# Kernel tuning notes

Hardware: AMD Instinct MI355X
Metric: run time of the kernel (lower is better)

Reference implementation:

```python
import jax, jax.numpy as jnp
import numpy as np

N_NODES = 50000
N_EDGES = 1600000
N_GRAPHS = 512
IN_SIZE = 44
HIDDEN = 256
CONV_NUMS = 3


def setup_inputs() -> dict:
    key = jax.random.key(0)
    ks = jax.random.split(key, 10)
    h = jax.random.normal(ks[0], (N_NODES, IN_SIZE), dtype=jnp.float32)
    src = jax.random.randint(ks[1], (N_EDGES,), 0, N_NODES)
    dst = jax.random.randint(ks[2], (N_EDGES,), 0, N_NODES)
    graph_ids = jnp.sort(jax.random.randint(ks[3], (N_NODES,), 0, N_GRAPHS))
    # learned params (kaiming-ish scale)
    W_proj = jax.random.normal(ks[4], (IN_SIZE, HIDDEN), dtype=jnp.float32) * (2.0 / IN_SIZE) ** 0.5
    b_proj = jnp.zeros((HIDDEN,), dtype=jnp.float32)
    W_lin = jax.random.normal(ks[5], (HIDDEN, HIDDEN), dtype=jnp.float32) * (2.0 / HIDDEN) ** 0.5
    b_lin = jnp.zeros((HIDDEN,), dtype=jnp.float32)
    W_out = jax.random.normal(ks[6], (HIDDEN * CONV_NUMS, HIDDEN), dtype=jnp.float32) * (2.0 / (HIDDEN * CONV_NUMS)) ** 0.5
    b_out = jnp.zeros((HIDDEN,), dtype=jnp.float32)
    return {"h": h, "src": src, "dst": dst, "graph_ids": graph_ids,
            "W_proj": W_proj, "b_proj": b_proj, "W_lin": W_lin, "b_lin": b_lin,
            "W_out": W_out, "b_out": b_out}


def reference(h, src, dst, graph_ids, W_proj, b_proj, W_lin, b_lin, W_out, b_out):
    # initial projection
    h = h @ W_proj + b_proj  # [N, HIDDEN]
    # in-degree for mean aggregation (nodes with 0 in-edges get 0 aggregate)
    ones_e = jnp.ones((src.shape[0],), dtype=h.dtype)
    deg = jax.ops.segment_sum(ones_e, dst, num_segments=N_NODES)  # [N]
    inv_deg = jnp.where(deg > 0, 1.0 / jnp.maximum(deg, 1.0), 0.0)[:, None]
    outs = []
    for _ in range(CONV_NUMS):
        # DGL GINConv(mean, eps=0): h' = linear(h + mean_{u in N(v)} h_u)
        agg = jax.ops.segment_sum(h[src], dst, num_segments=N_NODES) * inv_deg
        h = (h + agg) @ W_lin + b_lin  # shared linear across layers
        outs.append(h)
    res = jnp.concatenate(outs, axis=1) @ W_out + b_out  # [N, HIDDEN]
    # dgl.mean_nodes: per-graph mean readout
    cnt = jax.ops.segment_sum(jnp.ones((N_NODES,), dtype=res.dtype), graph_ids, num_segments=N_GRAPHS)
    g_sum = jax.ops.segment_sum(res, graph_ids, num_segments=N_GRAPHS)
    return g_sum / jnp.maximum(cnt, 1.0)[:, None]
```

## Files before the change

### kernel.cpp

```cpp
#include <hip/hip_runtime.h>
#include <hip/hip_fp8.h>

#define N_NODES   50000
#define N_EDGES   1600000
#define N_GRAPHS  512
#define IN_SIZE   44
#define HIDDEN    256
#define CONV_NUMS 3
#define NBK       ((N_NODES + 255) / 256)
#define XK        48

typedef __attribute__((ext_vector_type(8))) short short8v;
typedef __attribute__((ext_vector_type(4))) float f32x4;

__device__ __forceinline__ float bf2f(unsigned short u) {
    return __uint_as_float(((unsigned int)u) << 16);
}
__device__ __forceinline__ unsigned short f2bf(float f) {
    unsigned int u = __float_as_uint(f);
    unsigned int r = (u + 0x7fffu + ((u >> 16) & 1u)) >> 16;
    return (unsigned short)r;
}

#if __has_builtin(__builtin_amdgcn_cvt_f32_fp8)
template <int SEL>
__device__ __forceinline__ float fp8tof(unsigned int w) {
    return __builtin_amdgcn_cvt_f32_fp8((int)w, SEL);
}
#else
template <int SEL>
__device__ __forceinline__ float fp8tof(unsigned int w) {
    __hip_fp8_e4m3 q;
    q.__x = (__hip_fp8_storage_t)((w >> (SEL * 8)) & 0xff);
    return (float)q;
}
#endif

#if __has_builtin(__builtin_amdgcn_cvt_pk_fp8_f32)
__device__ __forceinline__ unsigned int pk4fp8(float f0, float f1, float f2, float f3) {
    int lo = __builtin_amdgcn_cvt_pk_fp8_f32(f0, f1, 0, false);
    return (unsigned int)__builtin_amdgcn_cvt_pk_fp8_f32(f2, f3, lo, true);
}
#else
__device__ __forceinline__ unsigned int pk4fp8(float f0, float f1, float f2, float f3) {
    __hip_fp8_e4m3 a(f0), b(f1), c(f2), d(f3);
    return (unsigned int)a.__x | ((unsigned int)b.__x << 8) |
           ((unsigned int)c.__x << 16) | ((unsigned int)d.__x << 24);
}
#endif

__device__ __forceinline__ unsigned char f2fp8(float f) {
    return (unsigned char)(pk4fp8(f, 0.f, 0.f, 0.f) & 0xff);
}

__global__ __launch_bounds__(256) void k_passA(const int* __restrict__ dst,
                                               const int* __restrict__ gid,
                                               int* __restrict__ bucket_cnt,
                                               int* __restrict__ gcnt) {
    __shared__ int hb[NBK];
    __shared__ int hg[N_GRAPHS];
    int tid = threadIdx.x;
    for (int i = tid; i < NBK; i += 256) hb[i] = 0;
    for (int i = tid; i < N_GRAPHS; i += 256) hg[i] = 0;
    __syncthreads();
    int t = blockIdx.x * 256 + tid;
    int stride = gridDim.x * 256;
    for (int e = t; e < N_EDGES; e += stride) atomicAdd(&hb[dst[e] >> 8], 1);
    for (int v = t; v < N_NODES; v += stride) atomicAdd(&hg[gid[v]], 1);
    __syncthreads();
    for (int i = tid; i < NBK; i += 256) if (hb[i]) atomicAdd(&bucket_cnt[i], hb[i]);
    for (int i = tid; i < N_GRAPHS; i += 256) if (hg[i]) atomicAdd(&gcnt[i], hg[i]);
}

__global__ void k_bscan(const int* __restrict__ bucket_cnt, int* __restrict__ bucket_base,
                        int* __restrict__ bucket_cursor, int* __restrict__ row_ptr) {
    __shared__ int s[256];
    int t = threadIdx.x;
    int v = (t < NBK) ? bucket_cnt[t] : 0;
    s[t] = v;
    __syncthreads();
    for (int off = 1; off < 256; off <<= 1) {
        int a = (t >= off) ? s[t - off] : 0;
        __syncthreads();
        s[t] += a;
        __syncthreads();
    }
    if (t < NBK) {
        int base = s[t] - v;
        bucket_base[t] = base;
        bucket_cursor[t] = base;
    }
    if (t == 0) {
        bucket_base[NBK] = N_EDGES;
        row_ptr[N_NODES] = N_EDGES;
    }
}

#define BCH 8192
__global__ __launch_bounds__(256) void k_passB(const int* __restrict__ src,
                                               const int* __restrict__ dst,
                                               int* __restrict__ bucket_cursor,
                                               int* __restrict__ pairs) {
    __shared__ int hist[NBK];
    __shared__ int excl[NBK];
    __shared__ int cur[NBK];
    __shared__ int gbase[NBK];
    __shared__ int lp[BCH];
    __shared__ int sc[256];
    int tid = threadIdx.x;
    int e0 = blockIdx.x * BCH;
    int cnt = min(BCH, N_EDGES - e0);
    for (int i = tid; i < NBK; i += 256) hist[i] = 0;
    __syncthreads();
    for (int i = tid; i < cnt; i += 256) atomicAdd(&hist[dst[e0 + i] >> 8], 1);
    __syncthreads();
    int hv = (tid < NBK) ? hist[tid] : 0;
    sc[tid] = hv;
    __syncthreads();
    for (int off = 1; off < 256; off <<= 1) {
        int a = (tid >= off) ? sc[tid - off] : 0;
        __syncthreads();
        sc[tid] += a;
        __syncthreads();
    }
    if (tid < NBK) {
        excl[tid] = sc[tid] - hv;
        cur[tid]  = sc[tid] - hv;
    }
    __syncthreads();
    for (int i = tid; i < cnt; i += 256) {
        int d = dst[e0 + i];
        int b = d >> 8;
        int pos = atomicAdd(&cur[b], 1);
        lp[pos] = (b << 24) | ((d & 255) << 16) | src[e0 + i];
    }
    __syncthreads();
    if (tid < NBK && hist[tid] > 0)
        gbase[tid] = atomicAdd(&bucket_cursor[tid], hist[tid]);
    __syncthreads();
    for (int i = tid; i < cnt; i += 256) {
        int p = lp[i];
        int b = (p >> 24) & 0xff;
        pairs[gbase[b] + (i - excl[b])] = p;
    }
}

__global__ __launch_bounds__(256) void k_passC(const int* __restrict__ pairs,
                                               const int* __restrict__ bucket_base,
                                               int* __restrict__ row_ptr,
                                               unsigned short* __restrict__ colu) {
    __shared__ int hist[256];
    __shared__ int cur[256];
    __shared__ int sc[256];
    int b = blockIdx.x;
    int tid = threadIdx.x;
    int v0 = b << 8;
    int e0 = bucket_base[b], e1 = bucket_base[b + 1];
    hist[tid] = 0;
    __syncthreads();
    for (int i = e0 + tid; i < e1; i += 256) atomicAdd(&hist[(pairs[i] >> 16) & 0xff], 1);
    __syncthreads();
    int hv = hist[tid];
    sc[tid] = hv;
    __syncthreads();
    for (int off = 1; off < 256; off <<= 1) {
        int a = (tid >= off) ? sc[tid - off] : 0;
        __syncthreads();
        sc[tid] += a;
        __syncthreads();
    }
    int base = e0 + sc[tid] - hv;
    int v = v0 + tid;
    if (v < N_NODES) row_ptr[v] = base;
    cur[tid] = base;
    __syncthreads();
    for (int i = e0 + tid; i < e1; i += 256) {
        int p = pairs[i];
        int pos = atomicAdd(&cur[(p >> 16) & 0xff], 1);
        colu[pos] = (unsigned short)(p & 0xffff);
    }
}

__global__ __launch_bounds__(256) void k_prep(const float* __restrict__ Wl,
                                              const float* __restrict__ Wproj,
                                              const float* __restrict__ X,
                                              unsigned short* __restrict__ WlPack,
                                              unsigned short* __restrict__ WprojPack,
                                              unsigned short* __restrict__ Xb,
                                              unsigned char* __restrict__ Xb8) {
    int b = blockIdx.x;
    int tid = threadIdx.x;
    if (b < 32) {
        int i = b * 256 + tid;
        int kg = i >> 8, n = i & 255;
        short8v v;
#pragma unroll
        for (int j = 0; j < 8; j++) v[j] = (short)f2bf(Wl[(kg * 8 + j) * HIDDEN + n]);
        *(short8v*)(WlPack + (size_t)(kg * 256 + n) * 8) = v;
    } else if (b < 40) {
        int i = (b - 32) * 256 + tid;
        int kg = i >> 8, n = i & 255;
        short8v v;
#pragma unroll
        for (int j = 0; j < 8; j++) {
            int k = kg * 8 + j;
            v[j] = (k < IN_SIZE) ? (short)f2bf(Wproj[k * HIDDEN + n]) : (short)0;
        }
        *(short8v*)(WprojPack + (size_t)(kg * 256 + n) * 8) = v;
    } else {
        const int TOT = N_NODES * XK;
        int id0 = (b - 40) * 2048 + tid;
#pragma unroll
        for (int j = 0; j < 8; j++) {
            int id = id0 + j * 256;
            if (id < TOT) {
                int row = id / XK, c = id % XK;
                float val = (c < IN_SIZE) ? X[row * IN_SIZE + c] : 0.f;
                Xb[id]  = f2bf(val);
                Xb8[id] = f2fp8(val);
            }
        }
    }
}

__device__ __forceinline__ int rsplit(const int* rp, int s0, int len, int k) {
    if (k >= 8) return 64;
    int t = s0 + (int)(((long long)len * k) >> 3);
    int lo = 0, hi = 64;
    while (lo < hi) {
        int mid = (lo + hi) >> 1;
        if (rp[mid] < t) lo = mid + 1; else hi = mid;
    }
    return lo;
}

#define TLS 264
#define K1S 72
__global__ __launch_bounds__(512, 8) void k_layer1(const unsigned short* __restrict__ Xb,
                                                   const unsigned char* __restrict__ Xb8,
                                                   const int* __restrict__ row_ptr,
                                                   const unsigned short* __restrict__ colu,
                                                   const unsigned short* __restrict__ WprojPack,
                                                   const float* __restrict__ bp,
                                                   const unsigned short* __restrict__ WlPack,
                                                   const float* __restrict__ bl,
                                                   const int* __restrict__ gid,
                                                   unsigned short* __restrict__ hout,
                                                   unsigned char* __restrict__ hout8,
                                                   float* __restrict__ GsumL) {
    __shared__ unsigned short tl[64 * TLS];
    unsigned short* tl1 = tl;
    __shared__ float bpm[64];
    __shared__ int gl[64];
    __shared__ int rp[65];
    int tid = threadIdx.x;
    int w = tid >> 6, lane = tid & 63, quad = lane >> 4, l16 = lane & 15;
    int m0 = blockIdx.x * 64;

    if (tid < 65) rp[tid] = row_ptr[min(m0 + tid, N_NODES)];
    if (tid < 64) gl[tid] = (m0 + tid < N_NODES) ? gid[m0 + tid] : -1;
    __syncthreads();
    int s0 = rp[0], len = rp[64] - s0;
    int rlo = rsplit(rp, s0, len, w), rhi = rsplit(rp, s0, len, w + 1);

    for (int r = rlo; r < rhi; r++) {
        int v = m0 + r;
        float a0 = 0.f, a1 = 0.f;
        float val = 0.f;
        float mul = 1.f;
        if (v < N_NODES) {
            int s = rp[r], e = rp[r + 1];
            if (lane < XK) {
                int i = s;
                for (; i + 8 <= e; i += 8) {
                    int u0 = colu[i],     u1 = colu[i + 1];
                    int u2 = colu[i + 2], u3 = colu[i + 3];
                    int u4 = colu[i + 4], u5 = colu[i + 5];
                    int u6 = colu[i + 6], u7 = colu[i + 7];
                    unsigned int t0 = Xb8[u0 * XK + lane];
                    unsigned int t1 = Xb8[u1 * XK + lane];
                    unsigned int t2 = Xb8[u2 * XK + lane];
                    unsigned int t3 = Xb8[u3 * XK + lane];
                    unsigned int t4 = Xb8[u4 * XK + lane];
                    unsigned int t5 = Xb8[u5 * XK + lane];
                    unsigned int t6 = Xb8[u6 * XK + lane];
                    unsigned int t7 = Xb8[u7 * XK + lane];
                    a0 += (fp8tof<0>(t0) + fp8tof<0>(t1)) + (fp8tof<0>(t2) + fp8tof<0>(t3));
                    a1 += (fp8tof<0>(t4) + fp8tof<0>(t5)) + (fp8tof<0>(t6) + fp8tof<0>(t7));
                }
                for (; i + 2 <= e; i += 2) {
                    a0 += fp8tof<0>((unsigned int)Xb8[colu[i] * XK + lane]);
                    a1 += fp8tof<0>((unsigned int)Xb8[colu[i + 1] * XK + lane]);
                }
                if (i < e) a0 += fp8tof<0>((unsigned int)Xb8[colu[i] * XK + lane]);
            }
            float inv = 0.f;
            if (e > s) { inv = 1.0f / (float)(e - s); mul = 2.f; }
            float self = (lane < XK) ? bf2f(Xb[(size_t)v * XK + lane]) : 0.f;
            val = self + inv * (a0 + a1);
        }
        tl1[r * K1S + lane] = (lane < XK) ? f2bf(val) : (unsigned short)0;
        if (lane == 0) bpm[r] = mul;
    }
    __syncthreads();

    int n0 = w * 32;
    f32x4 acc[4][2];
#pragma unroll
    for (int mt = 0; mt < 4; mt++) {
        acc[mt][0] = (f32x4){0.f, 0.f, 0.f, 0.f};
        acc[mt][1] = (f32x4){0.f, 0.f, 0.f, 0.f};
    }
#pragma unroll
    for (int ks = 0; ks < 2; ks++) {
        int kg = ks * 4 + quad;
        short8v bfr0 = *(const short8v*)(WprojPack + (size_t)(kg * 256 + n0 + l16) * 8);
        short8v bfr1 = *(const short8v*)(WprojPack + (size_t)(kg * 256 + n0 + 16 + l16) * 8);
#pragma unroll
        for (int mt = 0; mt < 4; mt++) {
            short8v afr = *(const short8v*)(tl1 + (mt * 16 + l16) * K1S + ks * 32 + quad * 8);
            acc[mt][0] = __builtin_amdgcn_mfma_f32_16x16x32_bf16(afr, bfr0, acc[mt][0], 0, 0, 0);
            acc[mt][1] = __builtin_amdgcn_mfma_f32_16x16x32_bf16(afr, bfr1, acc[mt][1], 0, 0, 0);
        }
    }
    __syncthreads();
#pragma unroll
    for (int nt = 0; nt < 2; nt++) {
        int colg = n0 + nt * 16 + l16;
        float bb = bp[colg];
#pragma unroll
        for (int mt = 0; mt < 4; mt++)
#pragma unroll
            for (int r = 0; r < 4; r++) {
                int row = mt * 16 + quad * 4 + r;
                tl[row * TLS + colg] = f2bf(acc[mt][nt][r] + bb * bpm[row]);
            }
    }
    __syncthreads();

#pragma unroll
    for (int mt = 0; mt < 4; mt++) {
        acc[mt][0] = (f32x4){0.f, 0.f, 0.f, 0.f};
        acc[mt][1] = (f32x4){0.f, 0.f, 0.f, 0.f};
    }
#pragma unroll
    for (int ks = 0; ks < 8; ks++) {
        int kg = ks * 4 + quad;
        short8v bfr0 = *(const short8v*)(WlPack + (size_t)(kg * 256 + n0 + l16) * 8);
        short8v bfr1 = *(const short8v*)(WlPack + (size_t)(kg * 256 + n0 + 16 + l16) * 8);
#pragma unroll
        for (int mt = 0; mt < 4; mt++) {
            short8v afr = *(const short8v*)(tl + (mt * 16 + l16) * TLS + ks * 32 + quad * 8);
            acc[mt][0] = __builtin_amdgcn_mfma_f32_16x16x32_bf16(afr, bfr0, acc[mt][0], 0, 0, 0);
            acc[mt][1] = __builtin_amdgcn_mfma_f32_16x16x32_bf16(afr, bfr1, acc[mt][1], 0, 0, 0);
        }
    }
    __syncthreads();

#pragma unroll
    for (int nt = 0; nt < 2; nt++) {
        int colg = n0 + nt * 16 + l16;
        float bb = bl[colg];
#pragma unroll
        for (int mt = 0; mt < 4; mt++)
#pragma unroll
            for (int r = 0; r < 4; r++)
                tl[(mt * 16 + quad * 4 + r) * TLS + colg] = f2bf(acc[mt][nt][r] + bb);
    }
    __syncthreads();

    for (int i = tid; i < 64 * 64; i += 512) {
        int r = i >> 6, c4 = i & 63;
        int v = m0 + r;
        if (v < N_NODES) {
            ushort4 q = *(ushort4*)(tl + r * TLS + c4 * 4);
            ((ushort4*)hout)[(size_t)v * 64 + c4] = q;
            ((unsigned int*)hout8)[(size_t)v * 64 + c4] =
                pk4fp8(bf2f(q.x), bf2f(q.y), bf2f(q.z), bf2f(q.w));
        }
    }
    {
        int c = tid & 255;
        int r0 = (tid >> 8) * 32;
        float a2 = 0.f;
        int curg = gl[r0];
        for (int r = r0; r < r0 + 32; r++) {
            int g = gl[r];
            if (g < 0) break;
            if (g != curg) {
                atomicAdd(&GsumL[curg * HIDDEN + c], a2);
                a2 = 0.f;
                curg = g;
            }
            a2 += bf2f(tl[r * TLS + c]);
        }
        if (curg >= 0) atomicAdd(&GsumL[curg * HIDDEN + c], a2);
    }
}

__global__ __launch_bounds__(512, 8) void k_layer(const unsigned short* __restrict__ h,
                                                  const unsigned char* __restrict__ h8,
                                                  const int* __restrict__ row_ptr,
                                                  const unsigned short* __restrict__ colu,
                                                  const unsigned short* __restrict__ Wpack,
                                                  const float* __restrict__ bias,
                                                  const int* __restrict__ gid,
                                                  unsigned short* __restrict__ hout,
                                                  unsigned char* __restrict__ hout8,
                                                  int write8,
                                                  float* __restrict__ GsumL) {
    __shared__ unsigned short tl[64 * TLS];
    __shared__ int gl[64];
    __shared__ int rp[65];
    int tid = threadIdx.x;
    int w = tid >> 6, lane = tid & 63, quad = lane >> 4, l16 = lane & 15;
    int m0 = blockIdx.x * 64;

    if (tid < 65) rp[tid] = row_ptr[min(m0 + tid, N_NODES)];
    if (tid < 64) gl[tid] = (m0 + tid < N_NODES) ? gid[m0 + tid] : -1;
    __syncthreads();
    int s0 = rp[0], len = rp[64] - s0;
    int rlo = rsplit(rp, s0, len, w), rhi = rsplit(rp, s0, len, w + 1);

    const unsigned int* h8v = (const unsigned int*)h8;
    const ushort4* hv = (const ushort4*)h;
    for (int r = rlo; r < rhi; r++) {
        int v = m0 + r;
        float a0 = 0.f, a1 = 0.f, a2 = 0.f, a3 = 0.f;
        if (v < N_NODES) {
            int s = rp[r], e = rp[r + 1];
            int i = s;
            for (; i + 8 <= e; i += 8) {
                int u0 = colu[i],     u1 = colu[i + 1];
                int u2 = colu[i + 2], u3 = colu[i + 3];
                int u4 = colu[i + 4], u5 = colu[i + 5];
                int u6 = colu[i + 6], u7 = colu[i + 7];
                unsigned int p0 = h8v[(size_t)u0 * 64 + lane];
                unsigned int p1 = h8v[(size_t)u1 * 64 + lane];
                unsigned int p2 = h8v[(size_t)u2 * 64 + lane];
                unsigned int p3 = h8v[(size_t)u3 * 64 + lane];
                unsigned int p4 = h8v[(size_t)u4 * 64 + lane];
                unsigned int p5 = h8v[(size_t)u5 * 64 + lane];
                unsigned int p6 = h8v[(size_t)u6 * 64 + lane];
                unsigned int p7 = h8v[(size_t)u7 * 64 + lane];
                a0 += (fp8tof<0>(p0) + fp8tof<0>(p1)) + (fp8tof<0>(p2) + fp8tof<0>(p3))
                    + (fp8tof<0>(p4) + fp8tof<0>(p5)) + (fp8tof<0>(p6) + fp8tof<0>(p7));
                a1 += (fp8tof<1>(p0) + fp8tof<1>(p1)) + (fp8tof<1>(p2) + fp8tof<1>(p3))
                    + (fp8tof<1>(p4) + fp8tof<1>(p5)) + (fp8tof<1>(p6) + fp8tof<1>(p7));
                a2 += (fp8tof<2>(p0) + fp8tof<2>(p1)) + (fp8tof<2>(p2) + fp8tof<2>(p3))
                    + (fp8tof<2>(p4) + fp8tof<2>(p5)) + (fp8tof<2>(p6) + fp8tof<2>(p7));
                a3 += (fp8tof<3>(p0) + fp8tof<3>(p1)) + (fp8tof<3>(p2) + fp8tof<3>(p3))
                    + (fp8tof<3>(p4) + fp8tof<3>(p5)) + (fp8tof<3>(p6) + fp8tof<3>(p7));
            }
            for (; i + 4 <= e; i += 4) {
                int u0 = colu[i], u1 = colu[i + 1], u2 = colu[i + 2], u3 = colu[i + 3];
                unsigned int p0 = h8v[(size_t)u0 * 64 + lane];
                unsigned int p1 = h8v[(size_t)u1 * 64 + lane];
                unsigned int p2 = h8v[(size_t)u2 * 64 + lane];
                unsigned int p3 = h8v[(size_t)u3 * 64 + lane];
                a0 += (fp8tof<0>(p0) + fp8tof<0>(p1)) + (fp8tof<0>(p2) + fp8tof<0>(p3));
                a1 += (fp8tof<1>(p0) + fp8tof<1>(p1)) + (fp8tof<1>(p2) + fp8tof<1>(p3));
                a2 += (fp8tof<2>(p0) + fp8tof<2>(p1)) + (fp8tof<2>(p2) + fp8tof<2>(p3));
                a3 += (fp8tof<3>(p0) + fp8tof<3>(p1)) + (fp8tof<3>(p2) + fp8tof<3>(p3));
            }
            for (; i < e; i++) {
                unsigned int p = h8v[(size_t)colu[i] * 64 + lane];
                a0 += fp8tof<0>(p); a1 += fp8tof<1>(p);
                a2 += fp8tof<2>(p); a3 += fp8tof<3>(p);
            }
            float inv = (e > s) ? 1.0f / (float)(e - s) : 0.0f;
            ushort4 hs = hv[(size_t)v * 64 + lane];
            a0 = bf2f(hs.x) + inv * a0;
            a1 = bf2f(hs.y) + inv * a1;
            a2 = bf2f(hs.z) + inv * a2;
            a3 = bf2f(hs.w) + inv * a3;
        }
        ushort4 o;
        o.x = f2bf(a0); o.y = f2bf(a1); o.z = f2bf(a2); o.w = f2bf(a3);
        *(ushort4*)(tl + r * TLS + lane * 4) = o;
    }
    __syncthreads();

    int n0 = w * 32;
    f32x4 acc[4][2];
#pragma unroll
    for (int mt = 0; mt < 4; mt++) {
        acc[mt][0] = (f32x4){0.f, 0.f, 0.f, 0.f};
        acc[mt][1] = (f32x4){0.f, 0.f, 0.f, 0.f};
    }
#pragma unroll
    for (int ks = 0; ks < 8; ks++) {
        int kg = ks * 4 + quad;
        short8v bfr0 = *(const short8v*)(Wpack + (size_t)(kg * 256 + n0 + l16) * 8);
        short8v bfr1 = *(const short8v*)(Wpack + (size_t)(kg * 256 + n0 + 16 + l16) * 8);
#pragma unroll
        for (int mt = 0; mt < 4; mt++) {
            short8v afr = *(const short8v*)(tl + (mt * 16 + l16) * TLS + ks * 32 + quad * 8);
            acc[mt][0] = __builtin_amdgcn_mfma_f32_16x16x32_bf16(afr, bfr0, acc[mt][0], 0, 0, 0);
            acc[mt][1] = __builtin_amdgcn_mfma_f32_16x16x32_bf16(afr, bfr1, acc[mt][1], 0, 0, 0);
        }
    }
    __syncthreads();

#pragma unroll
    for (int nt = 0; nt < 2; nt++) {
        int colg = n0 + nt * 16 + l16;
        float bb = bias[colg];
#pragma unroll
        for (int mt = 0; mt < 4; mt++)
#pragma unroll
            for (int r = 0; r < 4; r++)
                tl[(mt * 16 + quad * 4 + r) * TLS + colg] = f2bf(acc[mt][nt][r] + bb);
    }
    __syncthreads();

    for (int i = tid; i < 64 * 64; i += 512) {
        int r = i >> 6, c4 = i & 63;
        int v = m0 + r;
        if (v < N_NODES) {
            ushort4 q = *(ushort4*)(tl + r * TLS + c4 * 4);
            ((ushort4*)hout)[(size_t)v * 64 + c4] = q;
            if (write8)
                ((unsigned int*)hout8)[(size_t)v * 64 + c4] =
                    pk4fp8(bf2f(q.x), bf2f(q.y), bf2f(q.z), bf2f(q.w));
        }
    }
    {
        int c = tid & 255;
        int r0 = (tid >> 8) * 32;
        float a2 = 0.f;
        int curg = gl[r0];
        for (int r = r0; r < r0 + 32; r++) {
            int g = gl[r];
            if (g < 0) break;
            if (g != curg) {
                atomicAdd(&GsumL[curg * HIDDEN + c], a2);
                a2 = 0.f;
                curg = g;
            }
            a2 += bf2f(tl[r * TLS + c]);
        }
        if (curg >= 0) atomicAdd(&GsumL[curg * HIDDEN + c], a2);
    }
}

__global__ __launch_bounds__(256) void k_out(const float* __restrict__ Gsum,
                                             const int* __restrict__ gcnt,
                                             const float* __restrict__ Wout,
                                             const float* __restrict__ bout,
                                             float* __restrict__ out) {
    int g = blockIdx.x;
    int c = threadIdx.x;
    __shared__ float gm[HIDDEN * CONV_NUMS];
    float invc = 1.0f / fmaxf((float)gcnt[g], 1.0f);
    for (int i = c; i < HIDDEN * CONV_NUMS; i += 256) {
        int l = i >> 8;
        int k = i & 255;
        gm[i] = Gsum[(size_t)l * N_GRAPHS * HIDDEN + g * HIDDEN + k] * invc;
    }
    __syncthreads();
    float acc = bout[c];
    const float4* gm4 = (const float4*)gm;
    for (int k0 = 0; k0 < HIDDEN * CONV_NUMS; k0 += 4) {
        float4 gv = gm4[k0 >> 2];
        acc += gv.x * Wout[(k0 + 0) * HIDDEN + c];
        acc += gv.y * Wout[(k0 + 1) * HIDDEN + c];
        acc += gv.z * Wout[(k0 + 2) * HIDDEN + c];
        acc += gv.w * Wout[(k0 + 3) * HIDDEN + c];
    }
    out[g * HIDDEN + c] = acc;
}

extern "C" void kernel_launch(void* const* d_in, const int* in_sizes, int n_in,
                              void* d_out, int out_size, void* d_ws, size_t ws_size,
                              hipStream_t stream) {
    const float* X    = (const float*)d_in[0];
    const int*   src  = (const int*)d_in[1];
    const int*   dst  = (const int*)d_in[2];
    const int*   gid  = (const int*)d_in[3];
    const float* Wp   = (const float*)d_in[4];
    const float* bp   = (const float*)d_in[5];
    const float* Wl   = (const float*)d_in[6];
    const float* bl   = (const float*)d_in[7];
    const float* Wout = (const float*)d_in[8];
    const float* bout = (const float*)d_in[9];
    float* out = (float*)d_out;

    char* ws = (char*)d_ws;
    size_t off = 0;
    auto alloc = [&](size_t bytes) {
        char* p = ws + off;
        off += (bytes + 255) & ~size_t(255);
        return p;
    };
    unsigned short* h         = (unsigned short*)alloc(sizeof(short) * N_NODES * HIDDEN);
    unsigned short* t         = (unsigned short*)alloc(sizeof(short) * N_NODES * HIDDEN);
    unsigned char*  h8a       = (unsigned char*)alloc((size_t)N_NODES * HIDDEN);
    unsigned char*  h8b       = (unsigned char*)alloc((size_t)N_NODES * HIDDEN);
    unsigned short* WlPack    = (unsigned short*)alloc(sizeof(short) * HIDDEN * HIDDEN);
    unsigned short* WprojPack = (unsigned short*)alloc(sizeof(short) * 8 * 256 * 8);
    unsigned short* Xb        = (unsigned short*)alloc(sizeof(short) * N_NODES * XK);
    unsigned char*  Xb8       = (unsigned char*)alloc((size_t)N_NODES * XK);
    int*   pairs   = (int*)alloc(sizeof(int) * N_EDGES);
    unsigned short* colu = (unsigned short*)alloc(sizeof(short) * N_EDGES);
    int*   row_ptr = (int*)alloc(sizeof(int) * (N_NODES + 1));
    int*   bucket_base   = (int*)alloc(sizeof(int) * (NBK + 1));
    int*   bucket_cursor = (int*)alloc(sizeof(int) * NBK);
    char*  zero0 = ws + off;
    int*   bucket_cnt = (int*)alloc(sizeof(int) * NBK);
    int*   gcnt       = (int*)alloc(sizeof(int) * N_GRAPHS);
    float* Gsum       = (float*)alloc(sizeof(float) * CONV_NUMS * N_GRAPHS * HIDDEN);
    size_t zero_bytes = (size_t)((char*)(Gsum + CONV_NUMS * N_GRAPHS * HIDDEN) - zero0);

    hipMemsetAsync(zero0, 0, zero_bytes, stream);

    k_passA<<<512, 256, 0, stream>>>(dst, gid, bucket_cnt, gcnt);
    k_bscan<<<1, 256, 0, stream>>>(bucket_cnt, bucket_base, bucket_cursor, row_ptr);
    k_passB<<<(N_EDGES + BCH - 1) / BCH, 256, 0, stream>>>(src, dst, bucket_cursor, pairs);
    {
        const int TOT = N_NODES * XK;
        int ncast = (TOT + 2047) / 2048;
        k_prep<<<40 + ncast, 256, 0, stream>>>(Wl, Wp, X, WlPack, WprojPack, Xb, Xb8);
    }
    k_passC<<<NBK, 256, 0, stream>>>(pairs, bucket_base, row_ptr, colu);

    k_layer1<<<(N_NODES + 63) / 64, 512, 0, stream>>>(
        Xb, Xb8, row_ptr, colu, WprojPack, bp, WlPack, bl, gid, h, h8a, Gsum);

    k_layer<<<(N_NODES + 63) / 64, 512, 0, stream>>>(
        h, h8a, row_ptr, colu, WlPack, bl, gid, t, h8b, 1,
        Gsum + (size_t)1 * N_GRAPHS * HIDDEN);

    k_layer<<<(N_NODES + 63) / 64, 512, 0, stream>>>(
        t, h8b, row_ptr, colu, WlPack, bl, gid, h, h8a, 0,
        Gsum + (size_t)2 * N_GRAPHS * HIDDEN);

    k_out<<<N_GRAPHS, 256, 0, stream>>>(Gsum, gcnt, Wout, bout, out);
}
```

Baseline: 372.9 us.

## Merge histogram and prep kernels, use packed fp8 converts, drop edge-balanced row split

Fuses the degree/graph histogram kernel with the weight and input packing kernel into one launch, saving a kernel launch and letting the two independent jobs overlap. The layer kernels now give each wave a fixed eight rows instead of using a binary-searched, edge-balanced row split, which removes the shared row-pointer staging and one barrier. This risks load imbalance between waves when degrees vary. The gather accumulation also switches to packed two-wide fp8-to-float conversions to cut conversion instruction count.

```diff
diff --git a/kernel.cpp b/kernel.cpp
--- a/kernel.cpp
+++ b/kernel.cpp
@@ -12,6 +12,7 @@
 
 typedef __attribute__((ext_vector_type(8))) short short8v;
 typedef __attribute__((ext_vector_type(4))) float f32x4;
+typedef __attribute__((ext_vector_type(2))) float f32x2;
 
 __device__ __forceinline__ float bf2f(unsigned short u) {
     return __uint_as_float(((unsigned int)u) << 16);
@@ -36,6 +37,21 @@
 }
 #endif
 
+#if __has_builtin(__builtin_amdgcn_cvt_pk_f32_fp8)
+template <int HI>
+__device__ __forceinline__ f32x2 pk2f(unsigned int w) {
+    return __builtin_amdgcn_cvt_pk_f32_fp8((int)w, HI != 0);
+}
+#else
+template <int HI>
+__device__ __forceinline__ f32x2 pk2f(unsigned int w) {
+    f32x2 r;
+    r.x = fp8tof<2 * HI>(w);
+    r.y = fp8tof<2 * HI + 1>(w);
+    return r;
+}
+#endif
+
 #if __has_builtin(__builtin_amdgcn_cvt_pk_fp8_f32)
 __device__ __forceinline__ unsigned int pk4fp8(float f0, float f1, float f2, float f3) {
     int lo = __builtin_amdgcn_cvt_pk_fp8_f32(f0, f1, 0, false);
@@ -53,23 +69,63 @@
     return (unsigned char)(pk4fp8(f, 0.f, 0.f, 0.f) & 0xff);
 }
 
-__global__ __launch_bounds__(256) void k_passA(const int* __restrict__ dst,
-                                               const int* __restrict__ gid,
-                                               int* __restrict__ bucket_cnt,
-                                               int* __restrict__ gcnt) {
-    __shared__ int hb[NBK];
-    __shared__ int hg[N_GRAPHS];
+__global__ __launch_bounds__(256) void k_build0(const int* __restrict__ dst,
+                                                const int* __restrict__ gid,
+                                                const float* __restrict__ Wl,
+                                                const float* __restrict__ Wproj,
+                                                const float* __restrict__ X,
+                                                int* __restrict__ bucket_cnt,
+                                                int* __restrict__ gcnt,
+                                                unsigned short* __restrict__ WlPack,
+                                                unsigned short* __restrict__ WprojPack,
+                                                unsigned short* __restrict__ Xb,
+                                                unsigned char* __restrict__ Xb8) {
+    int b = blockIdx.x;
     int tid = threadIdx.x;
-    for (int i = tid; i < NBK; i += 256) hb[i] = 0;
-    for (int i = tid; i < N_GRAPHS; i += 256) hg[i] = 0;
-    __syncthreads();
-    int t = blockIdx.x * 256 + tid;
-    int stride = gridDim.x * 256;
-    for (int e = t; e < N_EDGES; e += stride) atomicAdd(&hb[dst[e] >> 8], 1);
-    for (int v = t; v < N_NODES; v += stride) atomicAdd(&hg[gid[v]], 1);
-    __syncthreads();
-    for (int i = tid; i < NBK; i += 256) if (hb[i]) atomicAdd(&bucket_cnt[i], hb[i]);
-    for (int i = tid; i < N_GRAPHS; i += 256) if (hg[i]) atomicAdd(&gcnt[i], hg[i]);
+    if (b < 512) {
+        __shared__ int hb[NBK];
+        __shared__ int hg[N_GRAPHS];
+        for (int i = tid; i < NBK; i += 256) hb[i] = 0;
+        for (int i = tid; i < N_GRAPHS; i += 256) hg[i] = 0;
+        __syncthreads();
+        int t = b * 256 + tid;
+        int stride = 512 * 256;
+        for (int e = t; e < N_EDGES; e += stride) atomicAdd(&hb[dst[e] >> 8], 1);
+        for (int v = t; v < N_NODES; v += stride) atomicAdd(&hg[gid[v]], 1);
+        __syncthreads();
+        for (int i = tid; i < NBK; i += 256) if (hb[i]) atomicAdd(&bucket_cnt[i], hb[i]);
+        for (int i = tid; i < N_GRAPHS; i += 256) if (hg[i]) atomicAdd(&gcnt[i], hg[i]);
+    } else if (b < 544) {
+        int i = (b - 512) * 256 + tid;
+        int kg = i >> 8, n = i & 255;
+        short8v v;
+#pragma unroll
+        for (int j = 0; j < 8; j++) v[j] = (short)f2bf(Wl[(kg * 8 + j) * HIDDEN + n]);
+        *(short8v*)(WlPack + (size_t)(kg * 256 + n) * 8) = v;
+    } else if (b < 552) {
+        int i = (b - 544) * 256 + tid;
+        int kg = i >> 8, n = i & 255;
+        short8v v;
+#pragma unroll
+        for (int j = 0; j < 8; j++) {
+            int k = kg * 8 + j;
+            v[j] = (k < IN_SIZE) ? (short)f2bf(Wproj[k * HIDDEN + n]) : (short)0;
+        }
+        *(short8v*)(WprojPack + (size_t)(kg * 256 + n) * 8) = v;
+    } else {
+        const int TOT = N_NODES * XK;
+        int id0 = (b - 552) * 2048 + tid;
+#pragma unroll
+        for (int j = 0; j < 8; j++) {
+            int id = id0 + j * 256;
+            if (id < TOT) {
+                int row = id / XK, c = id % XK;
+                float val = (c < IN_SIZE) ? X[row * IN_SIZE + c] : 0.f;
+                Xb[id]  = f2bf(val);
+                Xb8[id] = f2fp8(val);
+            }
+        }
+    }
 }
 
 __global__ void k_bscan(const int* __restrict__ bucket_cnt, int* __restrict__ bucket_base,
@@ -179,59 +235,6 @@
         int pos = atomicAdd(&cur[(p >> 16) & 0xff], 1);
         colu[pos] = (unsigned short)(p & 0xffff);
     }
-}
-
-__global__ __launch_bounds__(256) void k_prep(const float* __restrict__ Wl,
-                                              const float* __restrict__ Wproj,
-                                              const float* __restrict__ X,
-                                              unsigned short* __restrict__ WlPack,
-                                              unsigned short* __restrict__ WprojPack,
-                                              unsigned short* __restrict__ Xb,
-                                              unsigned char* __restrict__ Xb8) {
-    int b = blockIdx.x;
-    int tid = threadIdx.x;
-    if (b < 32) {
-        int i = b * 256 + tid;
-        int kg = i >> 8, n = i & 255;
-        short8v v;
-#pragma unroll
-        for (int j = 0; j < 8; j++) v[j] = (short)f2bf(Wl[(kg * 8 + j) * HIDDEN + n]);
-        *(short8v*)(WlPack + (size_t)(kg * 256 + n) * 8) = v;
-    } else if (b < 40) {
-        int i = (b - 32) * 256 + tid;
-        int kg = i >> 8, n = i & 255;
-        short8v v;
-#pragma unroll
-        for (int j = 0; j < 8; j++) {
-            int k = kg * 8 + j;
-            v[j] = (k < IN_SIZE) ? (short)f2bf(Wproj[k * HIDDEN + n]) : (short)0;
-        }
-        *(short8v*)(WprojPack + (size_t)(kg * 256 + n) * 8) = v;
-    } else {
-        const int TOT = N_NODES * XK;
-        int id0 = (b - 40) * 2048 + tid;
-#pragma unroll
-        for (int j = 0; j < 8; j++) {
-            int id = id0 + j * 256;
-            if (id < TOT) {
-                int row = id / XK, c = id % XK;
-                float val = (c < IN_SIZE) ? X[row * IN_SIZE + c] : 0.f;
-                Xb[id]  = f2bf(val);
-                Xb8[id] = f2fp8(val);
-            }
-        }
-    }
-}
-
-__device__ __forceinline__ int rsplit(const int* rp, int s0, int len, int k) {
-    if (k >= 8) return 64;
-    int t = s0 + (int)(((long long)len * k) >> 3);
-    int lo = 0, hi = 64;
-    while (lo < hi) {
-        int mid = (lo + hi) >> 1;
-        if (rp[mid] < t) lo = mid + 1; else hi = mid;
-    }
-    return lo;
 }
 
 #define TLS 264
@@ -252,24 +255,18 @@
     unsigned short* tl1 = tl;
     __shared__ float bpm[64];
     __shared__ int gl[64];
-    __shared__ int rp[65];
     int tid = threadIdx.x;
     int w = tid >> 6, lane = tid & 63, quad = lane >> 4, l16 = lane & 15;
     int m0 = blockIdx.x * 64;
 
-    if (tid < 65) rp[tid] = row_ptr[min(m0 + tid, N_NODES)];
-    if (tid < 64) gl[tid] = (m0 + tid < N_NODES) ? gid[m0 + tid] : -1;
-    __syncthreads();
-    int s0 = rp[0], len = rp[64] - s0;
-    int rlo = rsplit(rp, s0, len, w), rhi = rsplit(rp, s0, len, w + 1);
-
-    for (int r = rlo; r < rhi; r++) {
+    for (int rr = 0; rr < 8; rr++) {
+        int r = w * 8 + rr;
         int v = m0 + r;
         float a0 = 0.f, a1 = 0.f;
         float val = 0.f;
         float mul = 1.f;
         if (v < N_NODES) {
-            int s = rp[r], e = rp[r + 1];
+            int s = row_ptr[v], e = row_ptr[v + 1];
             if (lane < XK) {
                 int i = s;
                 for (; i + 8 <= e; i += 8) {
@@ -302,6 +299,7 @@
         tl1[r * K1S + lane] = (lane < XK) ? f2bf(val) : (unsigned short)0;
         if (lane == 0) bpm[r] = mul;
     }
+    if (tid < 64) gl[tid] = (m0 + tid < N_NODES) ? gid[m0 + tid] : -1;
     __syncthreads();
 
     int n0 = w * 32;
@@ -411,24 +409,19 @@
                                                   float* __restrict__ GsumL) {
     __shared__ unsigned short tl[64 * TLS];
     __shared__ int gl[64];
-    __shared__ int rp[65];
     int tid = threadIdx.x;
     int w = tid >> 6, lane = tid & 63, quad = lane >> 4, l16 = lane & 15;
     int m0 = blockIdx.x * 64;
 
-    if (tid < 65) rp[tid] = row_ptr[min(m0 + tid, N_NODES)];
-    if (tid < 64) gl[tid] = (m0 + tid < N_NODES) ? gid[m0 + tid] : -1;
-    __syncthreads();
-    int s0 = rp[0], len = rp[64] - s0;
-    int rlo = rsplit(rp, s0, len, w), rhi = rsplit(rp, s0, len, w + 1);
-
     const unsigned int* h8v = (const unsigned int*)h8;
     const ushort4* hv = (const ushort4*)h;
-    for (int r = rlo; r < rhi; r++) {
+    for (int rr = 0; rr < 8; rr++) {
+        int r = w * 8 + rr;
         int v = m0 + r;
-        float a0 = 0.f, a1 = 0.f, a2 = 0.f, a3 = 0.f;
+        f32x2 A = {0.f, 0.f};
+        f32x2 B = {0.f, 0.f};
         if (v < N_NODES) {
-            int s = rp[r], e = rp[r + 1];
+            int s = row_ptr[v], e = row_ptr[v + 1];
             int i = s;
             for (; i + 8 <= e; i += 8) {
                 int u0 = colu[i],     u1 = colu[i + 1];
@@ -443,14 +436,10 @@
                 unsigned int p5 = h8v[(size_t)u5 * 64 + lane];
                 unsigned int p6 = h8v[(size_t)u6 * 64 + lane];
                 unsigned int p7 = h8v[(size_t)u7 * 64 + lane];
-                a0 += (fp8tof<0>(p0) + fp8tof<0>(p1)) + (fp8tof<0>(p2) + fp8tof<0>(p3))
-                    + (fp8tof<0>(p4) + fp8tof<0>(p5)) + (fp8tof<0>(p6) + fp8tof<0>(p7));
-                a1 += (fp8tof<1>(p0) + fp8tof<1>(p1)) + (fp8tof<1>(p2) + fp8tof<1>(p3))
-                    + (fp8tof<1>(p4) + fp8tof<1>(p5)) + (fp8tof<1>(p6) + fp8tof<1>(p7));
-                a2 += (fp8tof<2>(p0) + fp8tof<2>(p1)) + (fp8tof<2>(p2) + fp8tof<2>(p3))
-                    + (fp8tof<2>(p4) + fp8tof<2>(p5)) + (fp8tof<2>(p6) + fp8tof<2>(p7));
-                a3 += (fp8tof<3>(p0) + fp8tof<3>(p1)) + (fp8tof<3>(p2) + fp8tof<3>(p3))
-                    + (fp8tof<3>(p4) + fp8tof<3>(p5)) + (fp8tof<3>(p6) + fp8tof<3>(p7));
+                A += (pk2f<0>(p0) + pk2f<0>(p1)) + (pk2f<0>(p2) + pk2f<0>(p3))
+                   + (pk2f<0>(p4) + pk2f<0>(p5)) + (pk2f<0>(p6) + pk2f<0>(p7));
+                B += (pk2f<1>(p0) + pk2f<1>(p1)) + (pk2f<1>(p2) + pk2f<1>(p3))
+                   + (pk2f<1>(p4) + pk2f<1>(p5)) + (pk2f<1>(p6) + pk2f<1>(p7));
             }
             for (; i + 4 <= e; i += 4) {
                 int u0 = colu[i], u1 = colu[i + 1], u2 = colu[i + 2], u3 = colu[i + 3];
@@ -458,27 +447,26 @@
                 unsigned int p1 = h8v[(size_t)u1 * 64 + lane];
                 unsigned int p2 = h8v[(size_t)u2 * 64 + lane];
                 unsigned int p3 = h8v[(size_t)u3 * 64 + lane];
-                a0 += (fp8tof<0>(p0) + fp8tof<0>(p1)) + (fp8tof<0>(p2) + fp8tof<0>(p3));
-                a1 += (fp8tof<1>(p0) + fp8tof<1>(p1)) + (fp8tof<1>(p2) + fp8tof<1>(p3));
-                a2 += (fp8tof<2>(p0) + fp8tof<2>(p1)) + (fp8tof<2>(p2) + fp8tof<2>(p3));
-                a3 += (fp8tof<3>(p0) + fp8tof<3>(p1)) + (fp8tof<3>(p2) + fp8tof<3>(p3));
+                A += (pk2f<0>(p0) + pk2f<0>(p1)) + (pk2f<0>(p2) + pk2f<0>(p3));
+                B += (pk2f<1>(p0) + pk2f<1>(p1)) + (pk2f<1>(p2) + pk2f<1>(p3));
             }
             for (; i < e; i++) {
                 unsigned int p = h8v[(size_t)colu[i] * 64 + lane];
-                a0 += fp8tof<0>(p); a1 += fp8tof<1>(p);
-                a2 += fp8tof<2>(p); a3 += fp8tof<3>(p);
+                A += pk2f<0>(p);
+                B += pk2f<1>(p);
             }
             float inv = (e > s) ? 1.0f / (float)(e - s) : 0.0f;
             ushort4 hs = hv[(size_t)v * 64 + lane];
-            a0 = bf2f(hs.x) + inv * a0;
-            a1 = bf2f(hs.y) + inv * a1;
-            a2 = bf2f(hs.z) + inv * a2;
-            a3 = bf2f(hs.w) + inv * a3;
+            A.x = bf2f(hs.x) + inv * A.x;
+            A.y = bf2f(hs.y) + inv * A.y;
+            B.x = bf2f(hs.z) + inv * B.x;
+            B.y = bf2f(hs.w) + inv * B.y;
         }
         ushort4 o;
-        o.x = f2bf(a0); o.y = f2bf(a1); o.z = f2bf(a2); o.w = f2bf(a3);
+        o.x = f2bf(A.x); o.y = f2bf(A.y); o.z = f2bf(B.x); o.w = f2bf(B.y);
         *(ushort4*)(tl + r * TLS + lane * 4) = o;
     }
+    if (tid < 64) gl[tid] = (m0 + tid < N_NODES) ? gid[m0 + tid] : -1;
     __syncthreads();
 
     int n0 = w * 32;
@@ -614,14 +602,14 @@
 
     hipMemsetAsync(zero0, 0, zero_bytes, stream);
 
-    k_passA<<<512, 256, 0, stream>>>(dst, gid, bucket_cnt, gcnt);
-    k_bscan<<<1, 256, 0, stream>>>(bucket_cnt, bucket_base, bucket_cursor, row_ptr);
-    k_passB<<<(N_EDGES + BCH - 1) / BCH, 256, 0, stream>>>(src, dst, bucket_cursor, pairs);
     {
         const int TOT = N_NODES * XK;
         int ncast = (TOT + 2047) / 2048;
-        k_prep<<<40 + ncast, 256, 0, stream>>>(Wl, Wp, X, WlPack, WprojPack, Xb, Xb8);
-    }
+        k_build0<<<552 + ncast, 256, 0, stream>>>(dst, gid, Wl, Wp, X, bucket_cnt,
+                                                  gcnt, WlPack, WprojPack, Xb, Xb8);
+    }
+    k_bscan<<<1, 256, 0, stream>>>(bucket_cnt, bucket_base, bucket_cursor, row_ptr);
+    k_passB<<<(N_EDGES + BCH - 1) / BCH, 256, 0, stream>>>(src, dst, bucket_cursor, pairs);
     k_passC<<<NBK, 256, 0, stream>>>(pairs, bucket_base, row_ptr, colu);
 
     k_layer1<<<(N_NODES + 63) / 64, 512, 0, stream>>>(
```

New measurement: 362.6 us. -2.7%, faster.
